# Kernel tuning notes

Hardware: AMD Instinct MI355X
Metric: run time of the kernel (lower is better)

The kernel has to match this reference:

```python
import jax, jax.numpy as jnp
import numpy as np

SEG_LENS = (2048, 4096, 8192)
DIL_RATES = (1, 2, 4)
NUM_HEADS = 12
HEAD_DIM = 64
LN_EPS = 1e-5


def _dilated_attention(q, k, v):
    # q,k,v: [b, n, h, d]; heads partitioned across (segment, dilation) groups
    b, n, h, d = q.shape
    G = len(SEG_LENS)
    hg = h // G
    scale = d ** -0.5
    out = jnp.zeros_like(q)
    for i, (s, r) in enumerate(zip(SEG_LENS, DIL_RATES)):
        hmin = i * hg
        m = n // s                      # number of segments
        idx = jnp.arange(i % r, s, r)   # dilated positions within a segment, len = s // r
        def seg(t):
            # [b, n, hg, d] -> [b, m, s//r, hg, d]
            return t[:, :, hmin:hmin + hg, :].reshape(b, m, s, hg, d)[:, :, idx]
        qs, ks, vs = seg(q), seg(k), seg(v)
        scores = jnp.einsum('bmshd,bmthd->bmhst', qs, ks) * scale  # [b,m,hg,s/r,s/r]
        attn = jax.nn.softmax(scores, axis=-1)
        o = jnp.einsum('bmhst,bmthd->bmshd', attn, vs)              # [b,m,s/r,hg,d]
        pos = (jnp.arange(m)[:, None] * s + idx[None, :]).reshape(-1)
        out = out.at[:, pos, hmin:hmin + hg, :].set(o.reshape(b, -1, hg, d))
    return out


def setup_inputs() -> dict:
    key = jax.random.key(0)
    ks = jax.random.split(key, 4)
    E = NUM_HEADS * HEAD_DIM
    b, n = 1, 8192
    x = jax.random.normal(ks[0], (b, n, E), dtype=jnp.float32)
    w_qkv = jax.random.normal(ks[1], (3 * E, E), dtype=jnp.float32) * (E ** -0.5)
    b_qkv = jnp.zeros((3 * E,), dtype=jnp.float32)
    w_out = jax.random.normal(ks[2], (E, E), dtype=jnp.float32) * (E ** -0.5)
    b_out = jnp.zeros((E,), dtype=jnp.float32)
    ln_gamma = jnp.ones((E,), dtype=jnp.float32)
    ln_beta = jnp.zeros((E,), dtype=jnp.float32)
    return {'x': x, 'w_qkv': w_qkv, 'b_qkv': b_qkv, 'w_out': w_out,
            'b_out': b_out, 'ln_gamma': ln_gamma, 'ln_beta': ln_beta}


def reference(x, w_qkv, b_qkv, w_out, b_out, ln_gamma, ln_beta):
    b, n, E = x.shape
    qkv = x @ w_qkv.T + b_qkv
    q, k, v = jnp.split(qkv, 3, axis=-1)
    shp = (b, n, NUM_HEADS, HEAD_DIM)
    o = _dilated_attention(q.reshape(shp), k.reshape(shp), v.reshape(shp)).reshape(b, n, E)
    # MAGNETO: LayerNorm on attention output before out projection
    mu = jnp.mean(o, axis=-1, keepdims=True)
    var = jnp.mean(jnp.square(o - mu), axis=-1, keepdims=True)
    on = (o - mu) / jnp.sqrt(var + LN_EPS) * ln_gamma + ln_beta
    return on @ w_out.T + b_out
```

## Files before the change

kernel.cpp:

```cpp
#include <hip/hip_runtime.h>
#include <hip/hip_bf16.h>
#include <cstdint>
#include <cstddef>


typedef __attribute__((ext_vector_type(8))) short short8;
typedef __attribute__((ext_vector_type(4))) short short4_;
typedef __attribute__((ext_vector_type(4))) float float4_;
typedef __attribute__((ext_vector_type(16))) float floatx16;
typedef __attribute__((ext_vector_type(4))) int int4_;

#if __has_builtin(__builtin_amdgcn_exp2f)
#define EXP2(x) __builtin_amdgcn_exp2f(x)
#else
#define EXP2(x) exp2f(x)
#endif

__device__ __forceinline__ float bf2f(short s) {
    unsigned int u = ((unsigned int)(unsigned short)s) << 16;
    float f;
    __builtin_memcpy(&f, &u, 4);
    return f;
}
__device__ __forceinline__ short f2bf(float f) {
    unsigned int u;
    __builtin_memcpy(&u, &f, 4);
    u += 0x7fffu + ((u >> 16) & 1u);
    return (short)(u >> 16);
}
__device__ __forceinline__ short8 f8_to_bf8(const float* __restrict__ p) {
    float4_ a = *(const float4_*)(p);
    float4_ b = *(const float4_*)(p + 4);
    short8 r;
    r[0] = f2bf(a[0]); r[1] = f2bf(a[1]); r[2] = f2bf(a[2]); r[3] = f2bf(a[3]);
    r[4] = f2bf(b[0]); r[5] = f2bf(b[1]); r[6] = f2bf(b[2]); r[7] = f2bf(b[3]);
    return r;
}
__device__ __forceinline__ void gll16(const short* g, short* l) {
    __builtin_amdgcn_global_load_lds(
        (const __attribute__((address_space(1))) unsigned int*)g,
        (__attribute__((address_space(3))) unsigned int*)l, 16, 0, 0);
}
__device__ __forceinline__ int cvtpk(float lo, float hi) {
    int r;
    asm("v_cvt_pk_bf16_f32 %0, %1, %2" : "=v"(r) : "v"(lo), "v"(hi));
    return r;
}

#define LDT 72

__global__ __launch_bounds__(256) void cvt3(
    const float* __restrict__ a, int na, const float* __restrict__ b, int nb,
    const float* __restrict__ c, int nc,
    short* __restrict__ oa, short* __restrict__ ob, short* __restrict__ oc)
{
    int i = (blockIdx.x * 256 + threadIdx.x) * 8;
    if (i < na) {
        *(short8*)&oa[i] = f8_to_bf8(a + i);
    } else if (i < na + nb) {
        int j = i - na;
        *(short8*)&ob[j] = f8_to_bf8(b + j);
    } else {
        int j = i - na - nb;
        if (j < nc) *(short8*)&oc[j] = f8_to_bf8(c + j);
    }
}

template<int EPI>
__global__ __launch_bounds__(256) void gemm128(
    const short* __restrict__ A, int lda,
    const short* __restrict__ B,
    const float* __restrict__ bias,
    void* __restrict__ Cv,
    int N, int K)
{
    __shared__ short As[128 * 64];
    __shared__ short Bs[128 * 64];
    const int tid  = threadIdx.x;
    const int wave = tid >> 6, lane = tid & 63;
    const int quad = lane >> 4, l16 = lane & 15;
    const int wr = wave >> 1, wc = wave & 1;
    const int m0 = blockIdx.y * 128, n0 = blockIdx.x * 128;
    const int lrow   = lane >> 3;
    const int lchunk = (lane & 7) ^ lrow;

    const short* Abase = A + (size_t)(m0 + wave * 32 + lrow) * lda + lchunk * 8;
    const short* Bbase = B + (size_t)(n0 + wave * 32 + lrow) * (size_t)K + lchunk * 8;
    short* AsW = &As[(wave * 32) * 64];
    short* BsW = &Bs[(wave * 32) * 64];

    float4_ acc[4][4] = {};

    for (int k0 = 0; k0 < K; k0 += 64) {
        __syncthreads();
        #pragma unroll
        for (int i = 0; i < 4; i++) {
            gll16(Abase + (size_t)(i * 8) * lda + k0, AsW + (i * 8) * 64);
            gll16(Bbase + (size_t)(i * 8) * K   + k0, BsW + (i * 8) * 64);
        }
        __syncthreads();
        #pragma unroll
        for (int ks = 0; ks < 2; ks++) {
            short8 af[4], bf[4];
            const int ca = ((ks * 4 + quad) ^ (l16 & 7)) * 8;
            #pragma unroll
            for (int t = 0; t < 4; t++) {
                af[t] = *(const short8*)&As[(wr * 64 + t * 16 + l16) * 64 + ca];
                bf[t] = *(const short8*)&Bs[(wc * 64 + t * 16 + l16) * 64 + ca];
            }
            #pragma unroll
            for (int mt = 0; mt < 4; mt++)
                #pragma unroll
                for (int nt = 0; nt < 4; nt++)
                    acc[mt][nt] = __builtin_amdgcn_mfma_f32_16x16x32_bf16(
                        af[mt], bf[nt], acc[mt][nt], 0, 0, 0);
        }
    }

    #pragma unroll
    for (int nt = 0; nt < 4; nt++) {
        const int col = n0 + wc * 64 + nt * 16 + l16;
        const float bv = bias[col];
        if constexpr (EPI == 0) {
            short* C = (short*)Cv;
            const int g = col >> 8;
            #pragma unroll
            for (int mt = 0; mt < 4; mt++) {
                #pragma unroll
                for (int r = 0; r < 4; r++) {
                    int row = m0 + wr * 64 + mt * 16 + quad * 4 + r;
                    bool cov = (col >= 768) || (g == 0) ||
                               (g == 1 && (row & 1) == 1) ||
                               (g == 2 && (row & 3) == 2);
                    C[(size_t)row * N + col] = cov ? f2bf(acc[mt][nt][r] + bv) : (short)0;
                }
            }
        } else {
            float* C = (float*)Cv;
            #pragma unroll
            for (int mt = 0; mt < 4; mt++)
                #pragma unroll
                for (int r = 0; r < 4; r++) {
                    int row = m0 + wr * 64 + mt * 16 + quad * 4 + r;
                    C[(size_t)row * N + col] = acc[mt][nt][r] + bv;
                }
        }
    }
}

__global__ __launch_bounds__(256, 4) void dilated_attn(
    const short* __restrict__ qkv, short* __restrict__ obuf1,
    short* __restrict__ obuf2, float* __restrict__ lbuf)
{
    __shared__ short Ks[2 * 64 * 64];
    __shared__ short Vt[2 * 64 * LDT];

    const int bx = blockIdx.x;
    const int L  = (bx & 7) * 112 + (bx >> 3);
    const int qt   = L & 15;
    const int half = (L >> 4) & 1;
    const int sh   = L >> 5;

    int g, seg, s, rate, off0;
    if (sh < 16)      { g = 0; seg = sh >> 2;        s = 2048; rate = 1; off0 = 0; }
    else if (sh < 24) { g = 1; seg = (sh - 16) >> 2; s = 4096; rate = 2; off0 = 1; }
    else              { g = 2; seg = 0;              s = 8192; rate = 4; off0 = 2; }
    const int head = g * 4 + (sh & 3);

    const int tid  = threadIdx.x;
    const int wave = tid >> 6, lane = tid & 63;
    const int h = lane >> 5, l32 = lane & 31;
    const int srow = tid >> 2, scol = (tid & 3) * 16;

    const size_t bpos = (size_t)seg * s + off0
                      + (size_t)(qt * 128 + wave * 32) * rate;
    short8 aq[4];
    {
        const short* qsrc = qkv + (bpos + (size_t)l32 * rate) * 2304
                                + head * 64 + h * 8;
        #pragma unroll
        for (int kt = 0; kt < 4; kt++) {
            short8 q = *(const short8*)(qsrc + kt * 16);
            #pragma unroll
            for (int e = 0; e < 8; e++) q[e] = f2bf(bf2f(q[e]) * 0.1803368801111244f);
            aq[kt] = q;
        }
    }

    const int krow0  = wave * 8 + (lane >> 3);
    const int kchunk = (lane & 7) ^ (lane >> 3);
    const size_t kstep = (size_t)64 * rate * 2304;
    const size_t kq0 = (size_t)seg * s + off0 + (size_t)(half * 1024) * rate;
    const short* kg0 = qkv + (kq0 + (size_t)krow0 * rate) * 2304
                           + 768 + head * 64 + kchunk * 8;
    const short* kg1 = kg0 + (size_t)32 * rate * 2304;
    const short* vgp = qkv + (kq0 + (size_t)srow * rate) * 2304
                           + 1536 + head * 64 + scol;
    const int kofsA = (wave * 8) * 64;
    const int kofsB = kofsA + 32 * 64;
    const int vswz  = scol;

    gll16(kg0, &Ks[kofsA]);
    gll16(kg1, &Ks[kofsB]);
    kg0 += kstep; kg1 += kstep;
    short8 va0 = *(const short8*)(vgp);
    short8 va1 = *(const short8*)(vgp + 8);
    vgp += kstep;
    #pragma unroll
    for (int e = 0; e < 8; e++) Vt[(scol + e) * LDT + (srow ^ vswz)] = va0[e];
    #pragma unroll
    for (int e = 0; e < 8; e++) Vt[(scol + 8 + e) * LDT + (srow ^ vswz)] = va1[e];
    va0 = *(const short8*)(vgp);
    va1 = *(const short8*)(vgp + 8);
    vgp += kstep;

    float lsum = 0.f;
    floatx16 oacc[2] = {};

    for (int j = 0; j < 16; j++) {
        __syncthreads();
        if (j < 15) {
            const int nb = (j + 1) & 1;
            gll16(kg0, &Ks[nb * 4096 + kofsA]);
            gll16(kg1, &Ks[nb * 4096 + kofsB]);
            kg0 += kstep; kg1 += kstep;
            short* vt = &Vt[nb * 64 * LDT];
            #pragma unroll
            for (int e = 0; e < 8; e++) vt[(scol + e) * LDT + (srow ^ vswz)] = va0[e];
            #pragma unroll
            for (int e = 0; e < 8; e++) vt[(scol + 8 + e) * LDT + (srow ^ vswz)] = va1[e];
            if (j < 14) {
                va0 = *(const short8*)(vgp);
                va1 = *(const short8*)(vgp + 8);
                vgp += kstep;
            }
        }
        const short* kb = &Ks[(j & 1) * 4096];
        const short* vb = &Vt[(j & 1) * 64 * LDT];

        floatx16 sacc[2] = {};
        __builtin_amdgcn_s_setprio(1);
        #pragma unroll
        for (int kt = 0; kt < 4; kt++) {
            #pragma unroll
            for (int t = 0; t < 2; t++) {
                short8 ak = *(const short8*)&kb[(t * 32 + l32) * 64
                                                + (((kt * 2 + h) ^ (l32 & 7)) * 8)];
                sacc[t] = __builtin_amdgcn_mfma_f32_32x32x16_bf16(
                    ak, aq[kt], sacc[t], 0, 0, 0);
            }
        }
        __builtin_amdgcn_s_setprio(0);

        #pragma unroll
        for (int e = 0; e < 16; e++) {
            float pa_ = EXP2(sacc[0][e]);
            float pb_ = EXP2(sacc[1][e]);
            sacc[0][e] = pa_; sacc[1][e] = pb_;
            lsum += pa_ + pb_;
        }

        short8 pa[4];
        #pragma unroll
        for (int kt = 0; kt < 4; kt++) {
            const int t = kt >> 1, b = (kt & 1) * 8;
            int A1 = cvtpk(sacc[t][b + 0], sacc[t][b + 1]);
            int A2 = cvtpk(sacc[t][b + 2], sacc[t][b + 3]);
            int B1 = cvtpk(sacc[t][b + 4], sacc[t][b + 5]);
            int B2 = cvtpk(sacc[t][b + 6], sacc[t][b + 7]);
            asm volatile("v_permlane32_swap_b32 %0, %1" : "+v"(A1), "+v"(B1));
            asm volatile("v_permlane32_swap_b32 %0, %1" : "+v"(A2), "+v"(B2));
            int4_ w; w[0] = A1; w[1] = A2; w[2] = B1; w[3] = B2;
            __builtin_memcpy(&pa[kt], &w, 16);
        }

        __builtin_amdgcn_s_setprio(1);
        #pragma unroll
        for (int kt = 0; kt < 4; kt++) {
            #pragma unroll
            for (int dt = 0; dt < 2; dt++) {
                const int d = dt * 32 + l32;
                short8 bv = *(const short8*)&vb[d * LDT
                                                + ((kt ^ ((d >> 4) & 3)) * 16 + h * 8)];
                oacc[dt] = __builtin_amdgcn_mfma_f32_32x32x16_bf16(
                    pa[kt], bv, oacc[dt], 0, 0, 0);
            }
        }
        __builtin_amdgcn_s_setprio(0);
    }

    {
        short* obase = half ? obuf2 : obuf1;
        float* lb = lbuf + (size_t)half * 8192 * 12;
        float lt = lsum + __shfl_xor(lsum, 32, 64);
        #pragma unroll
        for (int m = 0; m < 4; m++) {
            #pragma unroll
            for (int r = 0; r < 4; r++) {
                const int ql = 4 * h + r + 8 * m;
                short* od = obase + (bpos + (size_t)ql * rate) * 768 + head * 64;
                od[l32]      = f2bf(oacc[0][m * 4 + r]);
                od[32 + l32] = f2bf(oacc[1][m * 4 + r]);
            }
        }
        if (lane < 32)
            lb[(bpos + (size_t)l32 * rate) * 12 + head] = lt;
    }
}

__global__ __launch_bounds__(256) void ln_inplace(
    short* __restrict__ qkv, const short* __restrict__ obuf1,
    const short* __restrict__ obuf2, const float* __restrict__ lbuf,
    const float* __restrict__ gamma, const float* __restrict__ beta)
{
    const int row  = blockIdx.x * 4 + (threadIdx.x >> 6);
    const int lane = threadIdx.x & 63;
    const short* s1 = obuf1 + (size_t)row * 768;
    const short* s2 = obuf2 + (size_t)row * 768;
    short* dst = qkv + (size_t)row * 2304;

    const int h1 = lane >> 3;
    const int h2 = 8 + (lane >> 4);
    const bool cov1 = (h1 < 4) || ((row & 1) == 1);
    const bool cov2 = ((row & 3) == 2);
    const float li1 = cov1
        ? 1.0f / (lbuf[row * 12 + h1] + lbuf[8192 * 12 + row * 12 + h1]) : 0.0f;
    const float li2 = cov2
        ? 1.0f / (lbuf[row * 12 + h2] + lbuf[8192 * 12 + row * 12 + h2]) : 0.0f;

    short8  a  = *(const short8*)&s1[lane * 8];
    short4_ b  = *(const short4_*)&s1[512 + lane * 4];
    short8  a2 = *(const short8*)&s2[lane * 8];
    short4_ b2 = *(const short4_*)&s2[512 + lane * 4];
    float v[12];
    #pragma unroll
    for (int e = 0; e < 8; e++)
        v[e] = cov1 ? (bf2f(a[e]) + bf2f(a2[e])) * li1 : 0.0f;
    #pragma unroll
    for (int e = 0; e < 4; e++)
        v[8 + e] = cov2 ? (bf2f(b[e]) + bf2f(b2[e])) * li2 : 0.0f;

    float sum = 0.f, sq = 0.f;
    #pragma unroll
    for (int e = 0; e < 12; e++) { sum += v[e]; sq += v[e] * v[e]; }
    #pragma unroll
    for (int off = 1; off < 64; off <<= 1) {
        sum += __shfl_xor(sum, off, 64);
        sq  += __shfl_xor(sq,  off, 64);
    }
    float mean = sum * (1.0f / 768.0f);
    float var  = sq * (1.0f / 768.0f) - mean * mean;
    float rstd = rsqrtf(var + 1e-5f);

    short8 o8; short4_ o4;
    #pragma unroll
    for (int e = 0; e < 8; e++)
        o8[e] = f2bf((v[e] - mean) * rstd * gamma[lane * 8 + e] + beta[lane * 8 + e]);
    #pragma unroll
    for (int e = 0; e < 4; e++)
        o4[e] = f2bf((v[8 + e] - mean) * rstd * gamma[512 + lane * 4 + e] + beta[512 + lane * 4 + e]);

    *(short8*)&dst[lane * 8] = o8;
    *(short4_*)&dst[512 + lane * 4] = o4;
}

extern "C" void kernel_launch(void* const* d_in, const int* in_sizes, int n_in,
                              void* d_out, int out_size, void* d_ws, size_t ws_size,
                              hipStream_t stream) {
    const float* x     = (const float*)d_in[0];
    const float* w_qkv = (const float*)d_in[1];
    const float* b_qkv = (const float*)d_in[2];
    const float* w_out = (const float*)d_in[3];
    const float* b_out = (const float*)d_in[4];
    const float* gamma = (const float*)d_in[5];
    const float* beta  = (const float*)d_in[6];
    float* out = (float*)d_out;

    const int NX = 8192 * 768, NW1 = 2304 * 768, NW2 = 768 * 768;
    char* ws = (char*)d_ws;
    short* qkv   = (short*)(ws);
    short* xb    = (short*)(ws + (size_t)8192 * 2304 * 2);
    short* wqkvb = xb + NX;
    short* woutb = wqkvb + NW1;
    float* lbuf  = (float*)(woutb + NW2);
    short* obuf2 = (short*)(lbuf + 2 * 8192 * 12);
    short* obuf1 = xb;

    cvt3<<<dim3((NX + NW1 + NW2) / (256 * 8)), 256, 0, stream>>>(
        x, NX, w_qkv, NW1, w_out, NW2, xb, wqkvb, woutb);

    gemm128<0><<<dim3(2304 / 128, 8192 / 128), 256, 0, stream>>>(
        xb, 768, wqkvb, b_qkv, qkv, 2304, 768);

    dilated_attn<<<dim3(28 * 2 * 16), 256, 0, stream>>>(qkv, obuf1, obuf2, lbuf);

    ln_inplace<<<dim3(8192 / 4), 256, 0, stream>>>(
        qkv, obuf1, obuf2, lbuf, gamma, beta);

    gemm128<1><<<dim3(768 / 128, 8192 / 128), 256, 0, stream>>>(
        qkv, 2304, woutb, b_out, out, 768, 768);
}
```

Measured before the change: 207.7 us.

## Compute only dilated-selected rows in QKV projection with grouped block mapping

Replaces the dense QKV GEMM with a kernel that computes, for each head group, only the rows that the dilated attention actually reads (every row, every 2nd, every 4th), cutting the matmul work for groups 1 and 2. Blocks are remapped across a 1D grid of 672 tiles with an interleaved ordering, and A rows are gathered with a stride. Rows that are never computed are no longer zero-filled, so correctness now depends on downstream kernels not reading them. Strided row loads may reduce memory coalescing efficiency.

```diff
diff --git a/kernel.cpp b/kernel.cpp
--- a/kernel.cpp
+++ b/kernel.cpp
@@ -63,6 +63,83 @@
     } else {
         int j = i - na - nb;
         if (j < nc) *(short8*)&oc[j] = f8_to_bf8(c + j);
+    }
+}
+
+__global__ __launch_bounds__(256) void gemm_qkv(
+    const short* __restrict__ A,
+    const short* __restrict__ B,
+    const float* __restrict__ bias,
+    short* __restrict__ C)
+{
+    __shared__ short As[128 * 64];
+    __shared__ short Bs[128 * 64];
+
+    const int bx = blockIdx.x;
+    const int L  = (bx & 7) * 84 + (bx >> 3);
+    int g, t, rate, off0;
+    if (L < 384)      { g = 0; t = L;       rate = 1; off0 = 0; }
+    else if (L < 576) { g = 1; t = L - 384; rate = 2; off0 = 1; }
+    else              { g = 2; t = L - 576; rate = 4; off0 = 2; }
+    const int nx = t % 6, my = t / 6;
+    const int ncol0 = (nx >> 1) * 768 + g * 256 + (nx & 1) * 128;
+    const int m0 = my * 128;
+
+    const int tid  = threadIdx.x;
+    const int wave = tid >> 6, lane = tid & 63;
+    const int quad = lane >> 4, l16 = lane & 15;
+    const int wr = wave >> 1, wc = wave & 1;
+    const int lrow   = lane >> 3;
+    const int lchunk = (lane & 7) ^ lrow;
+
+    const short* Abase = A + (size_t)(off0 + (m0 + wave * 32 + lrow) * rate) * 768
+                           + lchunk * 8;
+    const short* Bbase = B + (size_t)(ncol0 + wave * 32 + lrow) * 768 + lchunk * 8;
+    short* AsW = &As[(wave * 32) * 64];
+    short* BsW = &Bs[(wave * 32) * 64];
+    const size_t arowstep = (size_t)8 * rate * 768;
+
+    float4_ acc[4][4] = {};
+
+    for (int k0 = 0; k0 < 768; k0 += 64) {
+        __syncthreads();
+        #pragma unroll
+        for (int i = 0; i < 4; i++) {
+            gll16(Abase + (size_t)i * arowstep + k0, AsW + (i * 8) * 64);
+            gll16(Bbase + (size_t)(i * 8) * 768 + k0, BsW + (i * 8) * 64);
+        }
+        __syncthreads();
+        #pragma unroll
+        for (int ks = 0; ks < 2; ks++) {
+            short8 af[4], bf[4];
+            const int ca = ((ks * 4 + quad) ^ (l16 & 7)) * 8;
+            #pragma unroll
+            for (int tt = 0; tt < 4; tt++) {
+                af[tt] = *(const short8*)&As[(wr * 64 + tt * 16 + l16) * 64 + ca];
+                bf[tt] = *(const short8*)&Bs[(wc * 64 + tt * 16 + l16) * 64 + ca];
+            }
+            #pragma unroll
+            for (int mt = 0; mt < 4; mt++)
+                #pragma unroll
+                for (int nt = 0; nt < 4; nt++)
+                    acc[mt][nt] = __builtin_amdgcn_mfma_f32_16x16x32_bf16(
+                        af[mt], bf[nt], acc[mt][nt], 0, 0, 0);
+        }
+    }
+
+    #pragma unroll
+    for (int nt = 0; nt < 4; nt++) {
+        const int gcol = ncol0 + wc * 64 + nt * 16 + l16;
+        const float bv = bias[gcol];
+        #pragma unroll
+        for (int mt = 0; mt < 4; mt++) {
+            #pragma unroll
+            for (int r = 0; r < 4; r++) {
+                const int rl = m0 + wr * 64 + mt * 16 + quad * 4 + r;
+                const size_t grow = (size_t)off0 + (size_t)rl * rate;
+                C[grow * 2304 + gcol] = f2bf(acc[mt][nt][r] + bv);
+            }
+        }
     }
 }
 
@@ -123,18 +200,13 @@
         const float bv = bias[col];
         if constexpr (EPI == 0) {
             short* C = (short*)Cv;
-            const int g = col >> 8;
-            #pragma unroll
-            for (int mt = 0; mt < 4; mt++) {
+            #pragma unroll
+            for (int mt = 0; mt < 4; mt++)
                 #pragma unroll
                 for (int r = 0; r < 4; r++) {
                     int row = m0 + wr * 64 + mt * 16 + quad * 4 + r;
-                    bool cov = (col >= 768) || (g == 0) ||
-                               (g == 1 && (row & 1) == 1) ||
-                               (g == 2 && (row & 3) == 2);
-                    C[(size_t)row * N + col] = cov ? f2bf(acc[mt][nt][r] + bv) : (short)0;
+                    C[(size_t)row * N + col] = f2bf(acc[mt][nt][r] + bv);
                 }
-            }
         } else {
             float* C = (float*)Cv;
             #pragma unroll
@@ -389,8 +461,7 @@
     cvt3<<<dim3((NX + NW1 + NW2) / (256 * 8)), 256, 0, stream>>>(
         x, NX, w_qkv, NW1, w_out, NW2, xb, wqkvb, woutb);
 
-    gemm128<0><<<dim3(2304 / 128, 8192 / 128), 256, 0, stream>>>(
-        xb, 768, wqkvb, b_qkv, qkv, 2304, 768);
+    gemm_qkv<<<dim3(672), 256, 0, stream>>>(xb, wqkvb, b_qkv, qkv);
 
     dilated_attn<<<dim3(28 * 2 * 16), 256, 0, stream>>>(qkv, obuf1, obuf2, lbuf);
 
```

New measurement: 193.6 us. 1.07x faster.
